# Optimization experiments

Measured on AMD Instinct MI355X. Metric: run time of the kernel, lower is better.

## Reference

```python
import math
import jax, jax.numpy as jnp
import numpy as np

NH, HD, CHUNK, PAST, FUT = 12, 128, 128, 127, 0  # heads, head_dim, chunk, left-1, right
CTX = CHUNK + PAST + FUT                          # 255
Q_SCALE = HD ** (-0.5) / math.log(2.0)
K_SCALE = math.log1p(math.e) / math.log(2.0)
SOFTCAP = 50.0


def setup_inputs() -> dict:
    key = jax.random.key(0)
    ks = jax.random.split(key, 8)
    B, S, H = 4, 4096, NH * HD
    return {
        "hidden_states": jax.random.normal(ks[0], (B, S, H), jnp.float32),
        "position_embeddings": jax.random.normal(ks[1], (CTX, H), jnp.float32),
        "Wq": jax.random.normal(ks[2], (H, H), jnp.float32) * 0.02,
        "Wk": jax.random.normal(ks[3], (H, H), jnp.float32) * 0.02,
        "Wv": jax.random.normal(ks[4], (H, H), jnp.float32) * 0.02,
        "Wrel": jax.random.normal(ks[5], (H, H), jnp.float32) * 0.02,
        "Wpost": jax.random.normal(ks[6], (H, H), jnp.float32) * 0.02,
        "per_dim_scale": jax.random.normal(ks[7], (HD,), jnp.float32) * 0.1,
    }


def reference(hidden_states, position_embeddings, Wq, Wk, Wv, Wrel, Wpost, per_dim_scale):
    B, S, H = hidden_states.shape
    # projections -> [B, S, nh, hd]; per-dim softplus scaling on queries (Gemma audio)
    q = (hidden_states @ Wq.T).reshape(B, S, NH, HD)
    q = q * (Q_SCALE * jax.nn.softplus(per_dim_scale))
    k = (hidden_states @ Wk.T).reshape(B, S, NH, HD) * K_SCALE
    v = (hidden_states @ Wv.T).reshape(B, S, NH, HD)

    NB = (S + CHUNK - 1) // CHUNK
    pad = NB * CHUNK - S
    q_blk = jnp.pad(q, ((0, 0), (0, pad), (0, 0), (0, 0))).reshape(B, NB, CHUNK, NH, HD)

    def extract_block_context(x):
        # pad [PAST] front, [FUT + CHUNK - 1] back; overlapping windows of CTX, stride CHUNK
        xp = jnp.pad(x, ((0, 0), (PAST, FUT + CHUNK - 1), (0, 0), (0, 0)))
        idx = jnp.arange(NB)[:, None] * CHUNK + jnp.arange(CTX)[None, :]  # [NB, CTX]
        return xp[:, idx]  # [B, NB, CTX, nh, hd]

    k_ctx = extract_block_context(k)
    v_ctx = extract_block_context(v)

    # content scores: [B, nh, NB, CHUNK, CTX]
    ac = jnp.einsum('bnchd,bnxhd->bhncx', q_blk, k_ctx)

    # relative-position scores with Transformer-XL style rel_shift
    rel_k = (position_embeddings @ Wrel.T).reshape(-1, NH, HD)  # [P, nh, hd]
    bd = jnp.einsum('bnchd,phd->bhncp', q_blk, rel_k)            # [B, nh, NB, CHUNK, P]
    P = bd.shape[-1]
    bd = jnp.pad(bd, ((0, 0), (0, 0), (0, 0), (0, 0), (0, CTX + 1 - P)))
    bd = bd.reshape(B, NH, NB, CHUNK * (CTX + 1))[..., : CHUNK * CTX]
    bd = bd.reshape(B, NH, NB, CHUNK, CTX)

    logits = SOFTCAP * jnp.tanh((ac + bd) / SOFTCAP)  # softcap
    w = jax.nn.softmax(logits, axis=-1)

    out = jnp.einsum('bhncx,bnxhd->bnchd', w, v_ctx)  # [B, NB, CHUNK, nh, hd]
    out = out.reshape(B, NB * CHUNK, NH * HD)[:, :S]
    return out @ Wpost.T
```

## Files before the change

### kernel.cpp

```cpp
#include <hip/hip_runtime.h>
#include <hip/hip_bf16.h>
#include <math.h>


#define NH_    12
#define HD_    128
#define H_     1536
#define B_     4
#define S_     4096
#define CHUNK_ 128
#define CTX_   255
#define NB_CH  32
#define QKW_   3072
#define BSTR_  4352

typedef unsigned short u16;
typedef short bf16x8 __attribute__((ext_vector_type(8)));
typedef float f32x4 __attribute__((ext_vector_type(4)));

static constexpr float Q_SCALE_F = (float)(0.08838834764831845 / 0.6931471805599453);
static constexpr float K_SCALE_F = (float)(1.3132616875182228 / 0.6931471805599453);

__device__ __forceinline__ u16 f2bf(float f) {
    __hip_bfloat16 h = __float2bfloat16(f);
    return __builtin_bit_cast(u16, h);
}
__device__ __forceinline__ float bf2f(u16 u) {
    unsigned int t = ((unsigned int)u) << 16;
    return __builtin_bit_cast(float, t);
}
__device__ __forceinline__ float fast_tanh(float t) {
    float u = __expf(-2.f * fabsf(t));
    float r = (1.f - u) / (1.f + u);
    return (t < 0.f) ? -r : r;
}

__device__ __forceinline__ void gload_lds16(const u16* src_global, u16* dst_lds) {
    __builtin_amdgcn_global_load_lds(
        (const __attribute__((address_space(1))) unsigned int*)src_global,
        (__attribute__((address_space(3))) unsigned int*)dst_lds,
        16, 0, 0);
}

__global__ __launch_bounds__(256)
void conv_bf16(const float* __restrict__ src, long long base,
               u16* __restrict__ dst, long long n,
               long long zero_below, long long zero_from,
               int mode, const float* __restrict__ pds, int ncols)
{
    long long i = ((long long)blockIdx.x * 256 + threadIdx.x) * 4;
    if (i >= n) return;
    float4 v = make_float4(0.f, 0.f, 0.f, 0.f);
    if (i >= zero_below && i < zero_from)
        v = *(const float4*)(src + base + i);
    float s = 1.f;
    if (mode == 1) {
        int row = (int)(i / ncols);
        float x = pds[row & 127];
        float sp = (x > 20.f) ? x : log1pf(__expf(x));
        s = Q_SCALE_F * sp;
    } else if (mode == 2) {
        s = K_SCALE_F;
    }
    ushort4 o = make_ushort4(f2bf(v.x * s), f2bf(v.y * s), f2bf(v.z * s), f2bf(v.w * s));
    *(ushort4*)(dst + i) = o;
}

__global__ __launch_bounds__(256)
void conv_hs(const float* __restrict__ src, long long src_row0,
             u16* __restrict__ dst, long long nelem)
{
    long long i = ((long long)blockIdx.x * 256 + threadIdx.x) * 4;
    if (i >= nelem) return;
    const int row = (int)(i / H_);
    const int col = (int)(i - (long long)row * H_);
    const int b = row / BSTR_;
    const int local = row - b * BSTR_;
    float4 v = make_float4(0.f, 0.f, 0.f, 0.f);
    if (local >= 128 && local < 128 + S_) {
        const long long srow = src_row0 + (long long)b * S_ + local - 128;
        v = *(const float4*)(src + srow * H_ + col);
    }
    ushort4 o = make_ushort4(f2bf(v.x), f2bf(v.y), f2bf(v.z), f2bf(v.w));
    *(ushort4*)(dst + i) = o;
}

#define STAGE(kt, bufc) do {                                                   \
    const int _ko = (kt) << 5;                                                 \
    gload_lds16(srcA[0] + _ko, lds + (bufc) * 4096 + pbase[0]);                \
    gload_lds16(srcA[1] + _ko, lds + (bufc) * 4096 + pbase[1]);                \
    gload_lds16(srcB[0] + _ko, lds + 16384 + (bufc) * 4096 + pbase[0]);        \
    gload_lds16(srcB[1] + _ko, lds + 16384 + (bufc) * 4096 + pbase[1]);        \
} while (0)

#define READF(afX, bfX, b) do {                                                \
    _Pragma("unroll")                                                          \
    for (int m = 0; m < 4; ++m)                                                \
        afX[m] = *(const bf16x8*)&lds[(b) * 4096 + (wr + m * 16 + lr) * 32 + sw8]; \
    _Pragma("unroll")                                                          \
    for (int n = 0; n < 4; ++n)                                                \
        bfX[n] = *(const bf16x8*)&lds[16384 + (b) * 4096 + (wc + n * 16 + lr) * 32 + sw8]; \
} while (0)

#define MFMA16(afX, bfX) do {                                                  \
    __builtin_amdgcn_s_setprio(1);                                             \
    _Pragma("unroll")                                                          \
    for (int m = 0; m < 4; ++m)                                                \
        _Pragma("unroll")                                                      \
        for (int n = 0; n < 4; ++n)                                            \
            acc[m][n] = __builtin_amdgcn_mfma_f32_16x16x32_bf16(afX[m], bfX[n], acc[m][n], 0, 0, 0); \
    __builtin_amdgcn_s_setprio(0);                                             \
} while (0)

#define ITER(t, b, afC, bfC, afN, bfN) do {                                    \
    if ((t) + 2 < nk) {                                                        \
        STAGE((t) + 2, ((b) + 2) & 3);                                         \
        asm volatile("s_waitcnt vmcnt(4)" ::: "memory");                       \
    } else {                                                                   \
        asm volatile("s_waitcnt vmcnt(0)" ::: "memory");                       \
    }                                                                          \
    __builtin_amdgcn_s_barrier();                                              \
    if ((t) + 1 < nk) READF(afN, bfN, ((b) + 1) & 3);                          \
    MFMA16(afC, bfC);                                                          \
} while (0)

__global__ __launch_bounds__(256)
void gemm_bt(const u16* __restrict__ A, const u16* __restrict__ B,
             u16* __restrict__ Cp, int M, int N, int K, int ldc)
{
    __shared__ __align__(16) u16 lds[32768];

    const int tid = threadIdx.x;
    const int w = tid >> 6, l = tid & 63;
    const int lr = l & 15, lg = l >> 4;
    const int bm = blockIdx.y * 128, bn = blockIdx.x * 128;
    const int wr = (w >> 1) * 64, wc = (w & 1) * 64;
    const int sw8 = (lg ^ ((lr >> 1) & 3)) * 8;

    const u16* srcA[2];
    const u16* srcB[2];
    int pbase[2];
#pragma unroll
    for (int c = 0; c < 2; ++c) {
        const int p = (w * 2 + c) * 64 + l;
        const int row = p >> 2;
        const int s_log = (p & 3) ^ ((row >> 1) & 3);
        pbase[c] = p * 8;
        srcA[c] = A + (size_t)(bm + row) * K + s_log * 8;
        srcB[c] = B + (size_t)(bn + row) * K + s_log * 8;
    }

    f32x4 acc[4][4];
#pragma unroll
    for (int m = 0; m < 4; ++m)
#pragma unroll
        for (int n = 0; n < 4; ++n) acc[m][n] = (f32x4){0.f, 0.f, 0.f, 0.f};

    const int nk = K >> 5;
    bf16x8 af0[4], bf0[4], af1[4], bf1[4];

    STAGE(0, 0);
    STAGE(1, 1);
    asm volatile("s_waitcnt vmcnt(4)" ::: "memory");
    __builtin_amdgcn_s_barrier();
    READF(af0, bf0, 0);

    for (int t0 = 0; t0 < nk; t0 += 4) {
        ITER(t0 + 0, 0, af0, bf0, af1, bf1);
        ITER(t0 + 1, 1, af1, bf1, af0, bf0);
        ITER(t0 + 2, 2, af0, bf0, af1, bf1);
        ITER(t0 + 3, 3, af1, bf1, af0, bf0);
    }

#pragma unroll
    for (int h = 0; h < 2; ++h) {
        if (wr == h * 64) {
#pragma unroll
            for (int m = 0; m < 4; ++m)
#pragma unroll
                for (int n = 0; n < 4; ++n)
#pragma unroll
                    for (int r = 0; r < 4; ++r)
                        lds[(m * 16 + lg * 4 + r) * 136 + wc + n * 16 + lr] =
                            f2bf(acc[m][n][r]);
        }
        __syncthreads();
#pragma unroll
        for (int it = 0; it < 4; ++it) {
            const int sid = it * 256 + tid;
            const int row = sid >> 4, sl = sid & 15;
            int4 val = *(const int4*)&lds[row * 136 + sl * 8];
            *(int4*)(Cp + (size_t)(bm + h * 64 + row) * ldc + bn + sl * 8) = val;
        }
        __syncthreads();
    }
}

#define STG2(kt, bufc) do {                                                    \
    const int _ko = (kt) << 5;                                                 \
    gload_lds16(srcA[0] + _ko, lds + (bufc) * 16384 + pbase[0]);               \
    gload_lds16(srcA[1] + _ko, lds + (bufc) * 16384 + pbase[1]);               \
    gload_lds16(srcB[0] + _ko, lds + (bufc) * 16384 + 8192 + pbase[0]);        \
    gload_lds16(srcB[1] + _ko, lds + (bufc) * 16384 + 8192 + pbase[1]);        \
} while (0)

#define IT2(t, b) do {                                                         \
    if ((t) + 2 < nk) {                                                        \
        STG2((t) + 2, ((b) + 2) & 3);                                          \
        asm volatile("s_waitcnt vmcnt(8)" ::: "memory");                       \
    } else if ((t) + 2 == nk) {                                                \
        asm volatile("s_waitcnt vmcnt(4)" ::: "memory");                       \
    } else {                                                                   \
        asm volatile("s_waitcnt vmcnt(0)" ::: "memory");                       \
    }                                                                          \
    __builtin_amdgcn_s_barrier();                                              \
    bf16x8 af[8], bfr[4];                                                      \
    _Pragma("unroll")                                                          \
    for (int m = 0; m < 8; ++m)                                                \
        af[m] = *(const bf16x8*)&lds[(b) * 16384 + (mbase + m * 16 + lr) * 32 + sw8]; \
    _Pragma("unroll")                                                          \
    for (int n = 0; n < 4; ++n)                                                \
        bfr[n] = *(const bf16x8*)&lds[(b) * 16384 + 8192 + (nbase + n * 16 + lr) * 32 + sw8]; \
    __builtin_amdgcn_s_setprio(1);                                             \
    _Pragma("unroll")                                                          \
    for (int m = 0; m < 8; ++m)                                                \
        _Pragma("unroll")                                                      \
        for (int n = 0; n < 4; ++n)                                            \
            acc[m][n] = __builtin_amdgcn_mfma_f32_16x16x32_bf16(af[m], bfr[n], acc[m][n], 0, 0, 0); \
    __builtin_amdgcn_s_setprio(0);                                             \
} while (0)

template<int OUTB>
__global__ __launch_bounds__(512, 2)
void gemm256(const u16* __restrict__ A, const u16* __restrict__ B,
             void* __restrict__ Cp, int M, int N, int K, int ldc)
{
    __shared__ __align__(16) u16 lds[65536];

    const int tid = threadIdx.x;
    const int w = tid >> 6, l = tid & 63;
    const int lr = l & 15, lg = l >> 4;
    const int wrow = w >> 2, wcol = w & 3;
    const int bm = blockIdx.y * 256, bn = blockIdx.x * 256;
    const int mbase = wrow * 128;
    const int nbase = wcol * 64;
    const int sw8 = (lg ^ ((lr >> 1) & 3)) * 8;

    const u16* srcA[2];
    const u16* srcB[2];
    int pbase[2];
#pragma unroll
    for (int c = 0; c < 2; ++c) {
        const int p = c * 512 + tid;
        const int row = p >> 2;
        const int s_log = (p & 3) ^ ((row >> 1) & 3);
        pbase[c] = p * 8;
        srcA[c] = A + (size_t)(bm + row) * K + s_log * 8;
        srcB[c] = B + (size_t)(bn + row) * K + s_log * 8;
    }

    f32x4 acc[8][4];
#pragma unroll
    for (int m = 0; m < 8; ++m)
#pragma unroll
        for (int n = 0; n < 4; ++n) acc[m][n] = (f32x4){0.f, 0.f, 0.f, 0.f};

    const int nk = K >> 5;
    STG2(0, 0);
    STG2(1, 1);
    for (int t0 = 0; t0 < nk; t0 += 4) {
        IT2(t0 + 0, 0);
        IT2(t0 + 1, 1);
        IT2(t0 + 2, 2);
        IT2(t0 + 3, 3);
    }

    __syncthreads();

    if (OUTB) {
#pragma unroll
        for (int h = 0; h < 2; ++h) {
            if (wrow == h) {
#pragma unroll
                for (int m = 0; m < 8; ++m)
#pragma unroll
                    for (int n = 0; n < 4; ++n)
#pragma unroll
                        for (int r = 0; r < 4; ++r)
                            lds[(m * 16 + lg * 4 + r) * 264 + nbase + n * 16 + lr] =
                                f2bf(acc[m][n][r]);
            }
            __syncthreads();
#pragma unroll
            for (int it = 0; it < 8; ++it) {
                const int sid = it * 512 + tid;
                const int row = sid >> 5, sl = sid & 31;
                int4 val = *(const int4*)&lds[row * 264 + sl * 8];
                *(int4*)((u16*)Cp + (size_t)(bm + h * 128 + row) * ldc + bn + sl * 8) = val;
            }
            __syncthreads();
        }
    } else {
#pragma unroll
        for (int m = 0; m < 8; ++m)
#pragma unroll
            for (int n = 0; n < 4; ++n)
#pragma unroll
                for (int r = 0; r < 4; ++r) {
                    const int row = bm + mbase + m * 16 + lg * 4 + r;
                    const int col = bn + nbase + n * 16 + lr;
                    ((float*)Cp)[(size_t)row * ldc + col] = acc[m][n][r];
                }
    }
}

__global__ __launch_bounds__(512)
void attn_mfma(const u16* __restrict__ qk, const u16* __restrict__ vT,
               const u16* __restrict__ relk, u16* __restrict__ attn_out,
               int vld)
{
    __shared__ __align__(16) u16 kv_s[256 * 128];
    __shared__ __align__(16) u16 g_s[128 * 264];

    const int ln = blockIdx.x, h = blockIdx.y, bz = blockIdx.z;
    const int tid = threadIdx.x;
    const int w = tid >> 6, l = tid & 63;
    const int lr = l & 15, lg = l >> 4;
    const size_t qbase = (size_t)bz * BSTR_;
    const size_t qrow0 = qbase + (size_t)(ln + 1) * 128;

    bf16x8 qa[4];
    {
        const u16* qp = qk + (qrow0 + w * 16 + lr) * QKW_ + h * HD_ + lg * 8;
#pragma unroll
        for (int kk = 0; kk < 4; ++kk) qa[kk] = *(const bf16x8*)(qp + kk * 32);
    }

#pragma unroll
    for (int it = 0; it < 8; ++it) {
        const int p = it * 512 + tid;
        const int row = p >> 4;
        const int s_log = (p & 15) ^ (row & 15);
        gload_lds16(relk + (size_t)row * H_ + h * HD_ + s_log * 8, kv_s + p * 8);
    }
    __syncthreads();

    f32x4 sacc[16];
#pragma unroll
    for (int n = 0; n < 16; ++n) sacc[n] = (f32x4){0.f, 0.f, 0.f, 0.f};
#pragma unroll
    for (int n = 0; n < 16; ++n)
#pragma unroll
        for (int kk = 0; kk < 4; ++kk) {
            int row = n * 16 + lr;
            int sl = kk * 4 + lg;
            bf16x8 bfrag = *(const bf16x8*)&kv_s[row * 128 + ((sl ^ (row & 15)) << 3)];
            sacc[n] = __builtin_amdgcn_mfma_f32_16x16x32_bf16(qa[kk], bfrag, sacc[n], 0, 0, 0);
        }

    const int c = w * 16 + lg * 4;
#pragma unroll
    for (int n = 0; n < 16; ++n)
#pragma unroll
        for (int r = 0; r < 4; ++r)
            g_s[(c + r) * 264 + n * 16 + lr] = f2bf(sacc[n][r]);
    __syncthreads();

#pragma unroll
    for (int it = 0; it < 8; ++it) {
        const int p = it * 512 + tid;
        const int row = p >> 4;
        const int s_log = (p & 15) ^ (row & 15);
        gload_lds16(qk + (qbase + (size_t)(ln * 128 + 1 + row)) * QKW_ + 1536 + h * HD_ + s_log * 8,
                    kv_s + p * 8);
    }
    __syncthreads();

#pragma unroll
    for (int n = 0; n < 16; ++n) sacc[n] = (f32x4){0.f, 0.f, 0.f, 0.f};
#pragma unroll
    for (int n = 0; n < 16; ++n)
#pragma unroll
        for (int kk = 0; kk < 4; ++kk) {
            int row = n * 16 + lr;
            int sl = kk * 4 + lg;
            bf16x8 bfrag = *(const bf16x8*)&kv_s[row * 128 + ((sl ^ (row & 15)) << 3)];
            sacc[n] = __builtin_amdgcn_mfma_f32_16x16x32_bf16(qa[kk], bfrag, sacc[n], 0, 0, 0);
        }

#pragma unroll
    for (int n = 0; n < 16; ++n)
#pragma unroll
        for (int r = 0; r < 4; ++r) {
            int cc = c + r;
            int x = n * 16 + lr;
            float val;
            if (x == 255) {
                val = -1e30f;
            } else {
                int dx = x - cc;
                u16 bdu = (dx >= 0) ? g_s[cc * 264 + dx]
                                    : g_s[(cc - 1) * 264 + dx + 256];
                float t = (sacc[n][r] + bf2f(bdu)) * (1.f / 50.f);
                val = 50.f * fast_tanh(t);
            }
            sacc[n][r] = val;
        }

#pragma unroll
    for (int r = 0; r < 4; ++r) {
        float m = -1e30f;
#pragma unroll
        for (int n = 0; n < 16; ++n) m = fmaxf(m, sacc[n][r]);
#pragma unroll
        for (int off = 1; off < 16; off <<= 1) m = fmaxf(m, __shfl_xor(m, off, 16));
        float s = 0.f;
#pragma unroll
        for (int n = 0; n < 16; ++n) {
            float e = __expf(sacc[n][r] - m);
            sacc[n][r] = e;
            s += e;
        }
#pragma unroll
        for (int off = 1; off < 16; off <<= 1) s += __shfl_xor(s, off, 16);
        float inv = 1.f / s;
#pragma unroll
        for (int n = 0; n < 16; ++n) sacc[n][r] *= inv;
    }
    __syncthreads();

#pragma unroll
    for (int n = 0; n < 16; ++n)
#pragma unroll
        for (int r = 0; r < 4; ++r)
            g_s[(c + r) * 264 + n * 16 + lr] = f2bf(sacc[n][r]);

#pragma unroll
    for (int it = 0; it < 8; ++it) {
        const int p = it * 512 + tid;
        const int d = p >> 5;
        const int s_log = (p & 31) ^ (d & 15);
        gload_lds16(vT + (size_t)(h * HD_ + d) * vld + qbase + ln * 128 + 1 + s_log * 8,
                    kv_s + p * 8);
    }
    __syncthreads();

    f32x4 oacc[8];
#pragma unroll
    for (int n = 0; n < 8; ++n) oacc[n] = (f32x4){0.f, 0.f, 0.f, 0.f};
#pragma unroll
    for (int kk = 0; kk < 8; ++kk) {
        int prow = w * 16 + lr;
        bf16x8 pa = *(const bf16x8*)&g_s[prow * 264 + kk * 32 + lg * 8];
#pragma unroll
        for (int n = 0; n < 8; ++n) {
            int d = n * 16 + lr;
            int sl = kk * 4 + lg;
            bf16x8 vb = *(const bf16x8*)&kv_s[d * 256 + ((sl ^ (d & 15)) << 3)];
            oacc[n] = __builtin_amdgcn_mfma_f32_16x16x32_bf16(pa, vb, oacc[n], 0, 0, 0);
        }
    }

    __syncthreads();
#pragma unroll
    for (int n = 0; n < 8; ++n)
#pragma unroll
        for (int r = 0; r < 4; ++r)
            kv_s[(c + r) * 136 + n * 16 + lr] = f2bf(oacc[n][r]);
    __syncthreads();
#pragma unroll
    for (int it = 0; it < 4; ++it) {
        const int sid = it * 512 + tid;
        const int row = sid >> 4, sl = sid & 15;
        int4 val = *(const int4*)&kv_s[row * 136 + sl * 8];
        *(int4*)(attn_out + ((size_t)bz * S_ + (size_t)(ln * 128 + row)) * H_ + h * HD_ + sl * 8) = val;
    }
}

extern "C" void kernel_launch(void* const* d_in, const int* in_sizes, int n_in,
                              void* d_out, int out_size, void* d_ws, size_t ws_size,
                              hipStream_t stream)
{
    (void)in_sizes; (void)n_in; (void)out_size;

    const float* hs    = (const float*)d_in[0];
    const float* pos   = (const float*)d_in[1];
    const float* Wq    = (const float*)d_in[2];
    const float* Wk    = (const float*)d_in[3];
    const float* Wv    = (const float*)d_in[4];
    const float* Wrel  = (const float*)d_in[5];
    const float* Wpost = (const float*)d_in[6];
    const float* pds   = (const float*)d_in[7];
    float* out = (float*)d_out;

    const long long WW = (long long)H_ * H_;
    const long long POSN = 256LL * H_;
    const long long fixed_elems = 5 * WW + 2 * POSN;

    int NB = 0;
    const int cand[3] = {4, 2, 1};
    for (int ci = 0; ci < 3; ++ci) {
        const int nb = cand[ci];
        const long long R = (long long)nb * BSTR_;
        const long long seg = R * (H_ + QKW_ + H_) + (long long)nb * S_ * H_;
        if ((fixed_elems + seg) * 2 <= (long long)ws_size) { NB = nb; break; }
    }
    if (NB == 0) return;

    const long long R = (long long)NB * BSTR_;
    const int vld = (int)R;

    u16* wqkb   = (u16*)d_ws;
    u16* wvb    = wqkb + 2 * WW;
    u16* wpostb = wvb + WW;
    u16* wrelb  = wpostb + WW;
    u16* posb   = wrelb + WW;
    u16* relkb  = posb + POSN;
    u16* hsb    = relkb + POSN;
    u16* qkb    = hsb + R * H_;
    u16* vTb    = qkb + R * QKW_;
    u16* attb   = vTb + (long long)H_ * R;

    dim3 blk(256);
    const long long BIG = 1LL << 60;

    conv_bf16<<<dim3(WW / 1024), blk, 0, stream>>>(Wq, 0, wqkb,        WW, 0, BIG, 1, pds, H_);
    conv_bf16<<<dim3(WW / 1024), blk, 0, stream>>>(Wk, 0, wqkb + WW,   WW, 0, BIG, 2, nullptr, H_);
    conv_bf16<<<dim3(WW / 1024), blk, 0, stream>>>(Wv, 0, wvb,         WW, 0, BIG, 0, nullptr, H_);
    conv_bf16<<<dim3(WW / 1024), blk, 0, stream>>>(Wpost, 0, wpostb,   WW, 0, BIG, 0, nullptr, H_);
    conv_bf16<<<dim3(WW / 1024), blk, 0, stream>>>(Wrel, 0, wrelb,     WW, 0, BIG, 0, nullptr, H_);
    conv_bf16<<<dim3(POSN / 1024), blk, 0, stream>>>(pos, 0, posb, POSN, 0, 255LL * H_, 0, nullptr, H_);

    gemm_bt<<<dim3(H_ / 128, 2), blk, 0, stream>>>(posb, wrelb, relkb, 256, H_, H_, H_);

    const long long hn = R * H_;
    for (int s = 0; s < B_ / NB; ++s) {
        const long long row0 = (long long)s * NB * S_;

        conv_hs<<<dim3((unsigned)(hn / 1024)), blk, 0, stream>>>(hs, row0, hsb, hn);

        gemm256<1><<<dim3(QKW_ / 256, (unsigned)(R / 256)), dim3(512), 0, stream>>>(
            hsb, wqkb, qkb, (int)R, QKW_, H_, QKW_);

        gemm256<1><<<dim3((unsigned)(R / 256), H_ / 256), dim3(512), 0, stream>>>(
            wvb, hsb, vTb, H_, (int)R, H_, vld);

        attn_mfma<<<dim3(NB_CH, NH_, NB), dim3(512), 0, stream>>>(
            qkb, vTb, relkb, attb, vld);

        gemm256<0><<<dim3(H_ / 256, (unsigned)((long long)NB * S_ / 256)), dim3(512), 0, stream>>>(
            attb, wpostb, out + row0 * H_, (int)(NB * S_), H_, H_, H_);
    }
}
```

Baseline: 573.1 us.

## Restructure GEMM main loop to BK=64 double buffer with staged MFMA phases

Reworks the gemm256 mainloop. It moves from a 4-deep ring of 32-wide K tiles to a 2-buffer scheme with 64-wide K tiles, laid out as 128-row halves with an XOR swizzle over 8 slots. Each K step is split into four A-fragment phases separated by barriers, with B fragments loaded once per step, so waves stay in lockstep and LDS reads interleave with MFMA bursts. This aims to cut per-tile loop and barrier overhead and improve LDS read reuse, at the cost of shallower prefetch depth and more barriers per step.

```diff
diff --git a/kernel.cpp b/kernel.cpp
--- a/kernel.cpp
+++ b/kernel.cpp
@@ -196,38 +196,12 @@
     }
 }
 
-#define STG2(kt, bufc) do {                                                    \
-    const int _ko = (kt) << 5;                                                 \
-    gload_lds16(srcA[0] + _ko, lds + (bufc) * 16384 + pbase[0]);               \
-    gload_lds16(srcA[1] + _ko, lds + (bufc) * 16384 + pbase[1]);               \
-    gload_lds16(srcB[0] + _ko, lds + (bufc) * 16384 + 8192 + pbase[0]);        \
-    gload_lds16(srcB[1] + _ko, lds + (bufc) * 16384 + 8192 + pbase[1]);        \
-} while (0)
-
-#define IT2(t, b) do {                                                         \
-    if ((t) + 2 < nk) {                                                        \
-        STG2((t) + 2, ((b) + 2) & 3);                                          \
-        asm volatile("s_waitcnt vmcnt(8)" ::: "memory");                       \
-    } else if ((t) + 2 == nk) {                                                \
-        asm volatile("s_waitcnt vmcnt(4)" ::: "memory");                       \
-    } else {                                                                   \
-        asm volatile("s_waitcnt vmcnt(0)" ::: "memory");                       \
-    }                                                                          \
-    __builtin_amdgcn_s_barrier();                                              \
-    bf16x8 af[8], bfr[4];                                                      \
-    _Pragma("unroll")                                                          \
-    for (int m = 0; m < 8; ++m)                                                \
-        af[m] = *(const bf16x8*)&lds[(b) * 16384 + (mbase + m * 16 + lr) * 32 + sw8]; \
-    _Pragma("unroll")                                                          \
-    for (int n = 0; n < 4; ++n)                                                \
-        bfr[n] = *(const bf16x8*)&lds[(b) * 16384 + 8192 + (nbase + n * 16 + lr) * 32 + sw8]; \
-    __builtin_amdgcn_s_setprio(1);                                             \
-    _Pragma("unroll")                                                          \
-    for (int m = 0; m < 8; ++m)                                                \
-        _Pragma("unroll")                                                      \
-        for (int n = 0; n < 4; ++n)                                            \
-            acc[m][n] = __builtin_amdgcn_mfma_f32_16x16x32_bf16(af[m], bfr[n], acc[m][n], 0, 0, 0); \
-    __builtin_amdgcn_s_setprio(0);                                             \
+#define STGH2(kt, half, isB, bufo) do {                                        \
+    const size_t _off = (size_t)(kt) * 64 + (size_t)(half) * hK;               \
+    const u16* _s0 = (isB) ? srcB[0] : srcA[0];                                \
+    const u16* _s1 = (isB) ? srcB[1] : srcA[1];                                \
+    gload_lds16(_s0 + _off, lds + (bufo) + ((isB) ? 16384 : 0) + (half) * 8192 + pb0); \
+    gload_lds16(_s1 + _off, lds + (bufo) + ((isB) ? 16384 : 0) + (half) * 8192 + pb1); \
 } while (0)
 
 template<int OUTB>
@@ -242,21 +216,27 @@
     const int lr = l & 15, lg = l >> 4;
     const int wrow = w >> 2, wcol = w & 3;
     const int bm = blockIdx.y * 256, bn = blockIdx.x * 256;
-    const int mbase = wrow * 128;
-    const int nbase = wcol * 64;
-    const int sw8 = (lg ^ ((lr >> 1) & 3)) * 8;
+    const size_t hK = (size_t)128 * K;
+
+    const int abase = wrow * 8192 + lr * 64;
+    const int bbase = 16384 + (wcol >> 1) * 8192 + (wcol & 1) * 4096 + lr * 64;
+    const int sk0 = ((0 + lg) ^ (lr & 7)) * 8;
+    const int sk1 = ((4 + lg) ^ (lr & 7)) * 8;
 
     const u16* srcA[2];
     const u16* srcB[2];
-    int pbase[2];
-#pragma unroll
-    for (int c = 0; c < 2; ++c) {
-        const int p = c * 512 + tid;
-        const int row = p >> 2;
-        const int s_log = (p & 3) ^ ((row >> 1) & 3);
-        pbase[c] = p * 8;
-        srcA[c] = A + (size_t)(bm + row) * K + s_log * 8;
-        srcB[c] = B + (size_t)(bn + row) * K + s_log * 8;
+    int pb0, pb1;
+    {
+        const int p0 = tid, p1 = tid + 512;
+        const int r0 = p0 >> 3, r1 = p1 >> 3;
+        const int sl0 = (p0 & 7) ^ (r0 & 7);
+        const int sl1 = (p1 & 7) ^ (r1 & 7);
+        pb0 = p0 * 8;
+        pb1 = p1 * 8;
+        srcA[0] = A + (size_t)(bm + r0) * K + sl0 * 8;
+        srcA[1] = A + (size_t)(bm + r1) * K + sl1 * 8;
+        srcB[0] = B + (size_t)(bn + r0) * K + sl0 * 8;
+        srcB[1] = B + (size_t)(bn + r1) * K + sl1 * 8;
     }
 
     f32x4 acc[8][4];
@@ -265,14 +245,69 @@
 #pragma unroll
         for (int n = 0; n < 4; ++n) acc[m][n] = (f32x4){0.f, 0.f, 0.f, 0.f};
 
-    const int nk = K >> 5;
-    STG2(0, 0);
-    STG2(1, 1);
-    for (int t0 = 0; t0 < nk; t0 += 4) {
-        IT2(t0 + 0, 0);
-        IT2(t0 + 1, 1);
-        IT2(t0 + 2, 2);
-        IT2(t0 + 3, 3);
+    const int nk = K >> 6;
+
+    STGH2(0, 0, 0, 0); STGH2(0, 1, 0, 0);
+    STGH2(0, 0, 1, 0); STGH2(0, 1, 1, 0);
+
+    for (int t = 0; t < nk; ++t) {
+        const int bo  = (t & 1) << 15;
+        const int bo1 = bo ^ 32768;
+
+        if (t + 1 < nk) {
+            STGH2(t + 1, 0, 0, bo1); STGH2(t + 1, 1, 0, bo1);
+            STGH2(t + 1, 0, 1, bo1); STGH2(t + 1, 1, 1, bo1);
+            asm volatile("s_waitcnt vmcnt(8)" ::: "memory");
+        } else {
+            asm volatile("s_waitcnt vmcnt(0)" ::: "memory");
+        }
+        __builtin_amdgcn_s_barrier();
+
+        bf16x8 bfr[4][2];
+#pragma unroll
+        for (int n = 0; n < 4; ++n) {
+            bfr[n][0] = *(const bf16x8*)&lds[bo + bbase + n * 1024 + sk0];
+            bfr[n][1] = *(const bf16x8*)&lds[bo + bbase + n * 1024 + sk1];
+        }
+        {
+            bf16x8 af[2][2];
+#pragma unroll
+            for (int i = 0; i < 2; ++i) {
+                af[i][0] = *(const bf16x8*)&lds[bo + abase + i * 1024 + sk0];
+                af[i][1] = *(const bf16x8*)&lds[bo + abase + i * 1024 + sk1];
+            }
+            __builtin_amdgcn_s_setprio(1);
+#pragma unroll
+            for (int i = 0; i < 2; ++i)
+#pragma unroll
+                for (int n = 0; n < 4; ++n) {
+                    acc[i][n] = __builtin_amdgcn_mfma_f32_16x16x32_bf16(af[i][0], bfr[n][0], acc[i][n], 0, 0, 0);
+                    acc[i][n] = __builtin_amdgcn_mfma_f32_16x16x32_bf16(af[i][1], bfr[n][1], acc[i][n], 0, 0, 0);
+                }
+            __builtin_amdgcn_s_setprio(0);
+        }
+
+#pragma unroll
+        for (int q = 1; q < 4; ++q) {
+            __builtin_amdgcn_s_barrier();
+            bf16x8 af[2][2];
+#pragma unroll
+            for (int i = 0; i < 2; ++i) {
+                af[i][0] = *(const bf16x8*)&lds[bo + abase + (q * 2 + i) * 1024 + sk0];
+                af[i][1] = *(const bf16x8*)&lds[bo + abase + (q * 2 + i) * 1024 + sk1];
+            }
+            __builtin_amdgcn_s_setprio(1);
+#pragma unroll
+            for (int i = 0; i < 2; ++i)
+#pragma unroll
+                for (int n = 0; n < 4; ++n) {
+                    acc[q * 2 + i][n] = __builtin_amdgcn_mfma_f32_16x16x32_bf16(af[i][0], bfr[n][0], acc[q * 2 + i][n], 0, 0, 0);
+                    acc[q * 2 + i][n] = __builtin_amdgcn_mfma_f32_16x16x32_bf16(af[i][1], bfr[n][1], acc[q * 2 + i][n], 0, 0, 0);
+                }
+            __builtin_amdgcn_s_setprio(0);
+        }
+
+        __builtin_amdgcn_s_barrier();
     }
 
     __syncthreads();
@@ -287,7 +322,7 @@
                     for (int n = 0; n < 4; ++n)
 #pragma unroll
                         for (int r = 0; r < 4; ++r)
-                            lds[(m * 16 + lg * 4 + r) * 264 + nbase + n * 16 + lr] =
+                            lds[(m * 16 + lg * 4 + r) * 264 + (wcol * 64) + n * 16 + lr] =
                                 f2bf(acc[m][n][r]);
             }
             __syncthreads();
@@ -307,8 +342,8 @@
             for (int n = 0; n < 4; ++n)
 #pragma unroll
                 for (int r = 0; r < 4; ++r) {
-                    const int row = bm + mbase + m * 16 + lg * 4 + r;
-                    const int col = bn + nbase + n * 16 + lr;
+                    const int row = bm + wrow * 128 + m * 16 + lg * 4 + r;
+                    const int col = bn + wcol * 64 + n * 16 + lr;
                     ((float*)Cp)[(size_t)row * ldc + col] = acc[m][n][r];
                 }
     }
```

Result: slower. 611.5 us (+6.7%).

## Deepen GEMM prefetch to three stages and merge QK and V projections into one launch

Applied to the files above, without the earlier changes.

The GEMM mainloop now issues global-to-LDS loads three K-tiles ahead instead of two, using all four LDS buffers, with the vmcnt waits adjusted to match. The QK projection and the transposed V projection now run as a single kernel over a flattened grid, which removes one launch and lets blocks from both GEMMs fill the device together, avoiding a tail between them. Deeper prefetch keeps more loads in flight, but a stage is reused one iteration sooner, so the waitcnt and barrier ordering must still protect buffer reuse.

```diff
diff --git a/kernel.cpp b/kernel.cpp
--- a/kernel.cpp
+++ b/kernel.cpp
@@ -204,9 +204,11 @@
     gload_lds16(srcB[1] + _ko, lds + (bufc) * 16384 + 8192 + pbase[1]);        \
 } while (0)
 
-#define IT2(t, b) do {                                                         \
-    if ((t) + 2 < nk) {                                                        \
-        STG2((t) + 2, ((b) + 2) & 3);                                          \
+#define IT3(t, b) do {                                                         \
+    if ((t) + 3 < nk) {                                                        \
+        STG2((t) + 3, ((b) + 3) & 3);                                          \
+        asm volatile("s_waitcnt vmcnt(12)" ::: "memory");                      \
+    } else if ((t) + 3 == nk) {                                                \
         asm volatile("s_waitcnt vmcnt(8)" ::: "memory");                       \
     } else if ((t) + 2 == nk) {                                                \
         asm volatile("s_waitcnt vmcnt(4)" ::: "memory");                       \
@@ -231,17 +233,17 @@
 } while (0)
 
 template<int OUTB>
-__global__ __launch_bounds__(512, 2)
-void gemm256(const u16* __restrict__ A, const u16* __restrict__ B,
-             void* __restrict__ Cp, int M, int N, int K, int ldc)
-{
-    __shared__ __align__(16) u16 lds[65536];
-
+__device__ __forceinline__
+void gemm256_body(const u16* __restrict__ A, const u16* __restrict__ B,
+                  void* __restrict__ Cp, int N, int K, int ldc,
+                  int bx, int by, u16* lds)
+{
+    (void)N;
     const int tid = threadIdx.x;
     const int w = tid >> 6, l = tid & 63;
     const int lr = l & 15, lg = l >> 4;
     const int wrow = w >> 2, wcol = w & 3;
-    const int bm = blockIdx.y * 256, bn = blockIdx.x * 256;
+    const int bm = by * 256, bn = bx * 256;
     const int mbase = wrow * 128;
     const int nbase = wcol * 64;
     const int sw8 = (lg ^ ((lr >> 1) & 3)) * 8;
@@ -268,11 +270,12 @@
     const int nk = K >> 5;
     STG2(0, 0);
     STG2(1, 1);
+    STG2(2, 2);
     for (int t0 = 0; t0 < nk; t0 += 4) {
-        IT2(t0 + 0, 0);
-        IT2(t0 + 1, 1);
-        IT2(t0 + 2, 2);
-        IT2(t0 + 3, 3);
+        IT3(t0 + 0, 0);
+        IT3(t0 + 1, 1);
+        IT3(t0 + 2, 2);
+        IT3(t0 + 3, 3);
     }
 
     __syncthreads();
@@ -312,6 +315,32 @@
                     ((float*)Cp)[(size_t)row * ldc + col] = acc[m][n][r];
                 }
     }
+}
+
+__global__ __launch_bounds__(512, 2)
+void gemm256_dual(const u16* __restrict__ A1, const u16* __restrict__ B1,
+                  void* __restrict__ C1, int N1, int K1, int ldc1, int nx1,
+                  const u16* __restrict__ A2, const u16* __restrict__ B2,
+                  void* __restrict__ C2, int N2, int K2, int ldc2, int nx2,
+                  int nqk)
+{
+    __shared__ __align__(16) u16 lds[65536];
+    const int flat = blockIdx.x;
+    if (flat < nqk) {
+        gemm256_body<1>(A1, B1, C1, N1, K1, ldc1, flat % nx1, flat / nx1, lds);
+    } else {
+        const int local = flat - nqk;
+        gemm256_body<1>(A2, B2, C2, N2, K2, ldc2, local % nx2, local / nx2, lds);
+    }
+}
+
+template<int OUTB>
+__global__ __launch_bounds__(512, 2)
+void gemm256(const u16* __restrict__ A, const u16* __restrict__ B,
+             void* __restrict__ Cp, int N, int K, int ldc)
+{
+    __shared__ __align__(16) u16 lds[65536];
+    gemm256_body<OUTB>(A, B, Cp, N, K, ldc, blockIdx.x, blockIdx.y, lds);
 }
 
 __global__ __launch_bounds__(512)
@@ -534,21 +563,25 @@
     gemm_bt<<<dim3(H_ / 128, 2), blk, 0, stream>>>(posb, wrelb, relkb, 256, H_, H_, H_);
 
     const long long hn = R * H_;
+    const int nx1 = QKW_ / 256;
+    const int nqk = nx1 * (int)(R / 256);
+    const int nx2 = (int)(R / 256);
+    const int nvt = nx2 * (H_ / 256);
+
     for (int s = 0; s < B_ / NB; ++s) {
         const long long row0 = (long long)s * NB * S_;
 
         conv_hs<<<dim3((unsigned)(hn / 1024)), blk, 0, stream>>>(hs, row0, hsb, hn);
 
-        gemm256<1><<<dim3(QKW_ / 256, (unsigned)(R / 256)), dim3(512), 0, stream>>>(
-            hsb, wqkb, qkb, (int)R, QKW_, H_, QKW_);
-
-        gemm256<1><<<dim3((unsigned)(R / 256), H_ / 256), dim3(512), 0, stream>>>(
-            wvb, hsb, vTb, H_, (int)R, H_, vld);
+        gemm256_dual<<<dim3((unsigned)(nqk + nvt)), dim3(512), 0, stream>>>(
+            hsb, wqkb, qkb, QKW_, H_, QKW_, nx1,
+            wvb, hsb, vTb, (int)R, H_, vld, nx2,
+            nqk);
 
         attn_mfma<<<dim3(NB_CH, NH_, NB), dim3(512), 0, stream>>>(
             qkb, vTb, relkb, attb, vld);
 
         gemm256<0><<<dim3(H_ / 256, (unsigned)((long long)NB * S_ / 256)), dim3(512), 0, stream>>>(
-            attb, wpostb, out + row0 * H_, (int)(NB * S_), H_, H_, H_);
-    }
-}
+            attb, wpostb, out + row0 * H_, H_, H_, H_);
+    }
+}
```

Result: faster. 541.1 us (-5.6%).
